# Performance work log

Hardware: AMD Instinct MI355X
Metric: run time of the kernel (lower is better)

Reference implementation:

```python
import jax, jax.numpy as jnp
import numpy as np

EPS_BN = 1e-5
EPS_ATT = 1e-9

def conv1x1(x, w, b=None):
    # x: [B,C,N], w: [O,C] -> [B,O,N]
    y = jnp.einsum('oc,bcn->bon', w, x)
    if b is not None:
        y = y + b[None, :, None]
    return y

def batchnorm1d(x, g, b):
    # training-mode BN over (batch, N) per channel, biased variance
    mean = jnp.mean(x, axis=(0, 2), keepdims=True)
    var = jnp.mean((x - mean) ** 2, axis=(0, 2), keepdims=True)
    xh = (x - mean) * jax.lax.rsqrt(var + EPS_BN)
    return xh * g[None, :, None] + b[None, :, None]

def sa_layer(x, xyz_emb, wqk, wv, bv, wt, bt, bng, bnb):
    # x, xyz_emb: [B,C,N]
    x = x + xyz_emb
    q = jnp.einsum('dc,bcn->bdn', wqk, x)      # [B,C/4,N] (shared weight)
    k = jnp.einsum('dc,bcn->bdn', wqk, x)
    v = conv1x1(x, wv, bv)                      # [B,C,N]
    attn = jnp.einsum('bdn,bdm->bnm', q, k)     # [B,N,N]: rows=queries n, cols=keys m
    attn = jax.nn.softmax(attn, axis=-1)
    attn = attn / (EPS_ATT + jnp.sum(attn, axis=1, keepdims=True))  # L1 renorm over dim=1
    x_r = jnp.einsum('bcn,bnm->bcm', v, attn)   # [B,C,N]
    x_r = jax.nn.relu(batchnorm1d(conv1x1(x - x_r, wt, bt), bng, bnb))
    return x + x_r

def setup_inputs() -> dict:
    key = jax.random.key(0)
    ks = jax.random.split(key, 12)
    B, C, N = 4, 128, 4096
    s = lambda fan: 1.0 / np.sqrt(fan)
    return {
        'x': jax.random.normal(ks[0], (B, C, N), jnp.float32),
        'xyz': jax.random.uniform(ks[1], (B, N, 3), jnp.float32),
        'conv1_w': jax.random.normal(ks[2], (C, C), jnp.float32) * s(C),
        'bn1_g': jnp.ones((C,), jnp.float32),
        'bn1_b': jnp.zeros((C,), jnp.float32),
        'pos_w': jax.random.normal(ks[3], (C, 3), jnp.float32) * s(3),
        'pos_b': jnp.zeros((C,), jnp.float32),
        'sa_wqk': jax.random.normal(ks[4], (5, C // 4, C), jnp.float32) * s(C),
        'sa_wv': jax.random.normal(ks[5], (5, C, C), jnp.float32) * s(C),
        'sa_bv': jnp.zeros((5, C), jnp.float32),
        'sa_wt': jax.random.normal(ks[6], (5, C, C), jnp.float32) * s(C),
        'sa_bt': jnp.zeros((5, C), jnp.float32),
        'sa_bng': jnp.ones((5, C), jnp.float32),
        'sa_bnb': jnp.zeros((5, C), jnp.float32),
    }

def reference(x, xyz, conv1_w, bn1_g, bn1_b, pos_w, pos_b,
              sa_wqk, sa_wv, sa_bv, sa_wt, sa_bt, sa_bng, sa_bnb):
    xyz_t = jnp.transpose(xyz, (0, 2, 1))           # [B,3,N]
    xyz_emb = conv1x1(xyz_t, pos_w, pos_b)          # [B,C,N]
    h = jax.nn.relu(batchnorm1d(conv1x1(x, conv1_w), bn1_g, bn1_b))
    outs = []
    for i in range(5):
        h = sa_layer(h, xyz_emb, sa_wqk[i], sa_wv[i], sa_bv[i],
                     sa_wt[i], sa_bt[i], sa_bng[i], sa_bnb[i])
        outs.append(h)
    return jnp.concatenate(outs, axis=1)            # [B,5C,N]
```

## Files before the change

kernel.cpp:

```cpp
#include <hip/hip_runtime.h>

#define kB 4
#define kC 128
#define kN 4096
#define kD 32
#define kL 5
#define kCO 640
#define kL2E 1.4426950408889634f

typedef float f32x4 __attribute__((ext_vector_type(4)));
typedef short bf16x4 __attribute__((ext_vector_type(4)));
typedef short bf16x8 __attribute__((ext_vector_type(8)));
typedef unsigned u32;
typedef u32 u32x4 __attribute__((ext_vector_type(4)));
typedef unsigned short u16;

__device__ __forceinline__ float bf2f(u16 u) {
  unsigned v = ((unsigned)u) << 16;
  return __builtin_bit_cast(float, v);
}
__device__ __forceinline__ u16 f2bf(float f) {
  unsigned u = __builtin_bit_cast(unsigned, f);
  u += 0x7fffu + ((u >> 16) & 1u);
  return (u16)(u >> 16);
}
__device__ __forceinline__ void split2(float v, u16& hi, u16& lo) {
  hi = f2bf(v);
  lo = f2bf(v - bf2f(hi));
}
__device__ __forceinline__ float fexp2(float x) {
#if __has_builtin(__builtin_amdgcn_exp2f)
  return __builtin_amdgcn_exp2f(x);
#else
  return exp2f(x);
#endif
}
__device__ __forceinline__ void splitpair(float a, float b, u32& hw, u32& lw) {
  u32 ua = __builtin_bit_cast(u32, a), ub = __builtin_bit_cast(u32, b);
  u32 uam = ua & 0xffff0000u, ubm = ub & 0xffff0000u;
  hw = (ua >> 16) | ubm;
  float la = a - __builtin_bit_cast(float, uam);
  float lb = b - __builtin_bit_cast(float, ubm);
  lw = (__builtin_bit_cast(u32, la) >> 16) | (__builtin_bit_cast(u32, lb) & 0xffff0000u);
}
__device__ __forceinline__ f32x4 mfma3(bf16x8 ah, bf16x8 al, bf16x8 bh, bf16x8 bl, f32x4 c) {
  c = __builtin_amdgcn_mfma_f32_16x16x32_bf16(ah, bh, c, 0, 0, 0);
  c = __builtin_amdgcn_mfma_f32_16x16x32_bf16(ah, bl, c, 0, 0, 0);
  c = __builtin_amdgcn_mfma_f32_16x16x32_bf16(al, bh, c, 0, 0, 0);
  return c;
}

__global__ void sentinel_kernel(float* out, float val, int total) {
  int i = blockIdx.x * 256 + threadIdx.x;
  if (i < total) out[i] = val;
}

__global__ void cvt_split_kernel(const float* __restrict__ src, u16* __restrict__ dh,
                                 u16* __restrict__ dl, int count) {
  int i = blockIdx.x * 256 + threadIdx.x;
  if (i < count) {
    u16 h, l;
    split2(src[i], h, l);
    dh[i] = h;
    dl[i] = l;
  }
}

__global__ __launch_bounds__(256) void prep_kernel(
    const float* __restrict__ h, long hstride, long hoff,
    u16* __restrict__ xh, u16* __restrict__ xl) {
  __shared__ float t[32][33];
  int n0 = blockIdx.x * 32, c0 = blockIdx.y * 32, b = blockIdx.z;
  int tx = threadIdx.x & 31, ty = threadIdx.x >> 5;
#pragma unroll
  for (int i = 0; i < 4; ++i) {
    int c = c0 + ty + i * 8;
    t[ty + i * 8][tx] = h[(size_t)b * hstride + hoff + (size_t)c * kN + n0 + tx];
  }
  __syncthreads();
#pragma unroll
  for (int i = 0; i < 4; ++i) {
    int n = n0 + ty + i * 8, c = c0 + tx;
    u16 hh, ll;
    split2(t[tx][ty + i * 8], hh, ll);
    size_t idx = ((size_t)b * kN + n) * kC + c;
    xh[idx] = hh;
    xl[idx] = ll;
  }
}

__global__ __launch_bounds__(320) void qv_kernel(
    const u16* __restrict__ xh, const u16* __restrict__ xl,
    const u16* __restrict__ wqkh, const u16* __restrict__ wqkl,
    const u16* __restrict__ wvh, const u16* __restrict__ wvl,
    const float* __restrict__ bv,
    u16* __restrict__ Qh, u16* __restrict__ Ql,
    u16* __restrict__ Vph, u16* __restrict__ Vpl) {
  __shared__ float vt[4][2][16][17];
  int wave = threadIdx.x >> 6, lane = threadIdx.x & 63;
  int b = blockIdx.y;
  int n0 = blockIdx.x * 16;
  int col = lane & 15, g = lane >> 4;
  f32x4 acc[2] = {};
  const u16* xrh = xh + ((size_t)b * kN + n0 + col) * kC + g * 8;
  const u16* xrl = xl + ((size_t)b * kN + n0 + col) * kC + g * 8;
#pragma unroll
  for (int kk = 0; kk < 4; ++kk) {
    bf16x8 bh = *(const bf16x8*)(xrh + kk * 32);
    bf16x8 bl = *(const bf16x8*)(xrl + kk * 32);
#pragma unroll
    for (int i = 0; i < 2; ++i) {
      int ot = wave * 2 + i;
      size_t wi = (ot < 2) ? ((size_t)(ot * 16 + col) * kC) : ((size_t)((ot - 2) * 16 + col) * kC);
      const u16* wsh = (ot < 2) ? (wqkh + wi) : (wvh + wi);
      const u16* wsl = (ot < 2) ? (wqkl + wi) : (wvl + wi);
      bf16x8 ah = *(const bf16x8*)(wsh + kk * 32 + g * 8);
      bf16x8 al = *(const bf16x8*)(wsl + kk * 32 + g * 8);
      acc[i] = mfma3(ah, al, bh, bl, acc[i]);
    }
  }
  if (wave > 0) {
#pragma unroll
    for (int i = 0; i < 2; ++i) {
      int ct = wave * 2 + i - 2;
#pragma unroll
      for (int r = 0; r < 4; ++r)
        vt[wave - 1][i][4 * g + r][col] = acc[i][r] + bv[ct * 16 + 4 * g + r];
    }
  }
  __syncthreads();
  if (wave == 0) {
#pragma unroll
    for (int i = 0; i < 2; ++i) {
#pragma unroll
      for (int r = 0; r < 4; ++r) {
        int d = i * 16 + 4 * g + r;
        u16 hh, ll;
        split2(acc[i][r], hh, ll);
        size_t idx = ((size_t)b * kN + n0 + col) * kD + d;
        Qh[idx] = hh;
        Ql[idx] = ll;
      }
    }
  } else {
    int nt = n0 >> 5, p = (n0 >> 4) & 1;
#pragma unroll
    for (int i = 0; i < 2; ++i) {
      int ct = wave * 2 + i - 2;
      bf16x4 vh4, vl4;
#pragma unroll
      for (int j = 0; j < 4; ++j) {
        float v = vt[wave - 1][i][col][4 * g + j];
        u16 hh, ll;
        split2(v, hh, ll);
        vh4[j] = (short)hh;
        vl4[j] = (short)ll;
      }
      size_t base = ((((size_t)b * (kN / 32) + nt) * 8 + ct) * 64 + lane) * 8 + p * 4;
      *(bf16x4*)(Vph + base) = vh4;
      *(bf16x4*)(Vpl + base) = vl4;
    }
  }
}

__global__ __launch_bounds__(256) void pass1_kernel(
    const u16* __restrict__ Qh, const u16* __restrict__ Ql,
    float* __restrict__ rm2, float* __restrict__ rinv) {
  __shared__ float mxs[4][16], sms[4][16];
  int wave = threadIdx.x >> 6, lane = threadIdx.x & 63;
  int b = blockIdx.y;
  int n0 = blockIdx.x * 16;
  int col = lane & 15, g = lane >> 4;
  const u16* qbh = Qh + (size_t)b * kN * kD;
  const u16* qbl = Ql + (size_t)b * kN * kD;
  bf16x8 ah = *(const bf16x8*)(qbh + (size_t)(n0 + col) * kD + g * 8);
  bf16x8 al = *(const bf16x8*)(qbl + (size_t)(n0 + col) * kD + g * 8);
  float mx[4] = {-3.0e38f, -3.0e38f, -3.0e38f, -3.0e38f};
  float sm[4] = {0.f, 0.f, 0.f, 0.f};
#pragma unroll 1
  for (int m0 = wave * 16; m0 < kN; m0 += 64) {
    bf16x8 bh = *(const bf16x8*)(qbh + (size_t)(m0 + col) * kD + g * 8);
    bf16x8 bl = *(const bf16x8*)(qbl + (size_t)(m0 + col) * kD + g * 8);
    f32x4 s = {};
    s = mfma3(ah, al, bh, bl, s);
#pragma unroll
    for (int r = 0; r < 4; ++r) {
      float nm = fmaxf(mx[r], s[r]);
      sm[r] = sm[r] * fexp2((mx[r] - nm) * kL2E) + fexp2((s[r] - nm) * kL2E);
      mx[r] = nm;
    }
  }
#pragma unroll
  for (int o = 1; o < 16; o <<= 1) {
#pragma unroll
    for (int r = 0; r < 4; ++r) {
      float Mo = __shfl_xor(mx[r], o, 64);
      float So = __shfl_xor(sm[r], o, 64);
      float nm = fmaxf(mx[r], Mo);
      sm[r] = sm[r] * fexp2((mx[r] - nm) * kL2E) + So * fexp2((Mo - nm) * kL2E);
      mx[r] = nm;
    }
  }
  if (col == 0) {
#pragma unroll
    for (int r = 0; r < 4; ++r) {
      mxs[wave][4 * g + r] = mx[r];
      sms[wave][4 * g + r] = sm[r];
    }
  }
  __syncthreads();
  if (threadIdx.x < 16) {
    int t = threadIdx.x;
    float M = mxs[0][t], S = sms[0][t];
#pragma unroll
    for (int w = 1; w < 4; ++w) {
      float Mo = mxs[w][t], So = sms[w][t];
      float nm = fmaxf(M, Mo);
      S = S * fexp2((M - nm) * kL2E) + So * fexp2((Mo - nm) * kL2E);
      M = nm;
    }
    rm2[(size_t)b * kN + n0 + t] = M * kL2E;
    rinv[(size_t)b * kN + n0 + t] = 1.0f / S;
  }
}

__global__ __launch_bounds__(256) void pass2_kernel(
    const u16* __restrict__ Qh, const u16* __restrict__ Ql,
    const u16* __restrict__ Vph, const u16* __restrict__ Vpl,
    const float* __restrict__ rm2, const float* __restrict__ rinv,
    const u16* __restrict__ xh, const u16* __restrict__ xl,
    u16* __restrict__ yth, u16* __restrict__ ytl) {
  __shared__ f32x4 accs[4][8][64];
  __shared__ float csl[2][4][16];
  int wave = threadIdx.x >> 6, lane = threadIdx.x & 63;
  int b = blockIdx.y;
  int m0 = blockIdx.x * 32;
  int col = lane & 15, g = lane >> 4;
  const u16* qbh = Qh + (size_t)b * kN * kD;
  const u16* qbl = Ql + (size_t)b * kN * kD;
  const float* rmb = rm2 + (size_t)b * kN;
  const float* rib = rinv + (size_t)b * kN;
  bf16x8 bmh0 = *(const bf16x8*)(qbh + (size_t)(m0 + col) * kD + g * 8);
  bf16x8 bml0 = *(const bf16x8*)(qbl + (size_t)(m0 + col) * kD + g * 8);
  bf16x8 bmh1 = *(const bf16x8*)(qbh + (size_t)(m0 + 16 + col) * kD + g * 8);
  bf16x8 bml1 = *(const bf16x8*)(qbl + (size_t)(m0 + 16 + col) * kD + g * 8);
  const u16* vbh = Vph + (size_t)b * (kN / 32) * 4096;
  const u16* vbl = Vpl + (size_t)b * (kN / 32) * 4096;
  f32x4 accA[8] = {}, accB[8] = {};
  float csA = 0.f, csB = 0.f;
#pragma unroll 1
  for (int nn = wave * 32; nn < kN; nn += 128) {
    bf16x8 ah0 = *(const bf16x8*)(qbh + (size_t)(nn + col) * kD + g * 8);
    bf16x8 al0 = *(const bf16x8*)(qbl + (size_t)(nn + col) * kD + g * 8);
    bf16x8 ah1 = *(const bf16x8*)(qbh + (size_t)(nn + 16 + col) * kD + g * 8);
    bf16x8 al1 = *(const bf16x8*)(qbl + (size_t)(nn + 16 + col) * kD + g * 8);
    f32x4 sA0 = {}, sA1 = {}, sB0 = {}, sB1 = {};
    sA0 = mfma3(ah0, al0, bmh0, bml0, sA0);
    sA1 = mfma3(ah1, al1, bmh0, bml0, sA1);
    sB0 = mfma3(ah0, al0, bmh1, bml1, sB0);
    sB1 = mfma3(ah1, al1, bmh1, bml1, sB1);
    float pA[8], pB[8];
#pragma unroll
    for (int r = 0; r < 4; ++r) {
      float e0 = rmb[nn + 4 * g + r], i0 = rib[nn + 4 * g + r];
      float e1 = rmb[nn + 16 + 4 * g + r], i1 = rib[nn + 16 + 4 * g + r];
      pA[r] = fexp2(sA0[r] * kL2E - e0) * i0;
      pA[r + 4] = fexp2(sA1[r] * kL2E - e1) * i1;
      pB[r] = fexp2(sB0[r] * kL2E - e0) * i0;
      pB[r + 4] = fexp2(sB1[r] * kL2E - e1) * i1;
      csA += pA[r] + pA[r + 4];
      csB += pB[r] + pB[r + 4];
    }
    u32x4 Ahw, Alw, Bhw, Blw;
#pragma unroll
    for (int k2 = 0; k2 < 4; ++k2) {
      u32 h0, l0, h1, l1;
      splitpair(pA[2 * k2], pA[2 * k2 + 1], h0, l0);
      splitpair(pB[2 * k2], pB[2 * k2 + 1], h1, l1);
      Ahw[k2] = h0; Alw[k2] = l0;
      Bhw[k2] = h1; Blw[k2] = l1;
    }
    bf16x8 bAh = __builtin_bit_cast(bf16x8, Ahw);
    bf16x8 bAl = __builtin_bit_cast(bf16x8, Alw);
    bf16x8 bBh = __builtin_bit_cast(bf16x8, Bhw);
    bf16x8 bBl = __builtin_bit_cast(bf16x8, Blw);
    size_t vtile = (size_t)(nn >> 5) * 4096;
#pragma unroll
    for (int ct = 0; ct < 8; ++ct) {
      size_t off = vtile + ((size_t)ct * 64 + lane) * 8;
      bf16x8 a8h = *(const bf16x8*)(vbh + off);
      bf16x8 a8l = *(const bf16x8*)(vbl + off);
      accA[ct] = mfma3(a8h, a8l, bAh, bAl, accA[ct]);
      accB[ct] = mfma3(a8h, a8l, bBh, bBl, accB[ct]);
    }
  }
  csA += __shfl_xor(csA, 16, 64);
  csA += __shfl_xor(csA, 32, 64);
  csB += __shfl_xor(csB, 16, 64);
  csB += __shfl_xor(csB, 32, 64);
  if (lane < 16) {
    csl[0][wave][lane] = csA;
    csl[1][wave][lane] = csB;
  }
#pragma unroll
  for (int ct = 0; ct < 8; ++ct) accs[wave][ct][lane] = accA[ct];
  __syncthreads();
  {
    float inv = 1.0f / (1e-9f + csl[0][0][col] + csl[0][1][col] + csl[0][2][col] + csl[0][3][col]);
    const u16* xrh = xh + ((size_t)b * kN + m0 + col) * kC;
    const u16* xrl = xl + ((size_t)b * kN + m0 + col) * kC;
#pragma unroll
    for (int i = 0; i < 2; ++i) {
      int ct = wave * 2 + i;
      f32x4 a = accs[0][ct][lane];
      a += accs[1][ct][lane];
      a += accs[2][ct][lane];
      a += accs[3][ct][lane];
      bf16x4 xvh = *(const bf16x4*)(xrh + ct * 16 + 4 * g);
      bf16x4 xvl = *(const bf16x4*)(xrl + ct * 16 + 4 * g);
#pragma unroll
      for (int r = 0; r < 4; ++r) {
        float xv = bf2f((u16)xvh[r]) + bf2f((u16)xvl[r]);
        float y = xv - a[r] * inv;
        u16 hh, ll;
        split2(y, hh, ll);
        size_t idx = ((size_t)b * kN + m0 + col) * kC + ct * 16 + 4 * g + r;
        yth[idx] = hh;
        ytl[idx] = ll;
      }
    }
  }
  __syncthreads();
#pragma unroll
  for (int ct = 0; ct < 8; ++ct) accs[wave][ct][lane] = accB[ct];
  __syncthreads();
  {
    float inv = 1.0f / (1e-9f + csl[1][0][col] + csl[1][1][col] + csl[1][2][col] + csl[1][3][col]);
    const u16* xrh = xh + ((size_t)b * kN + m0 + 16 + col) * kC;
    const u16* xrl = xl + ((size_t)b * kN + m0 + 16 + col) * kC;
#pragma unroll
    for (int i = 0; i < 2; ++i) {
      int ct = wave * 2 + i;
      f32x4 a = accs[0][ct][lane];
      a += accs[1][ct][lane];
      a += accs[2][ct][lane];
      a += accs[3][ct][lane];
      bf16x4 xvh = *(const bf16x4*)(xrh + ct * 16 + 4 * g);
      bf16x4 xvl = *(const bf16x4*)(xrl + ct * 16 + 4 * g);
#pragma unroll
      for (int r = 0; r < 4; ++r) {
        float xv = bf2f((u16)xvh[r]) + bf2f((u16)xvl[r]);
        float y = xv - a[r] * inv;
        u16 hh, ll;
        split2(y, hh, ll);
        size_t idx = ((size_t)b * kN + m0 + 16 + col) * kC + ct * 16 + 4 * g + r;
        yth[idx] = hh;
        ytl[idx] = ll;
      }
    }
  }
}

__global__ __launch_bounds__(256) void tconv_kernel(
    const u16* __restrict__ inh, const u16* __restrict__ inl,
    const u16* __restrict__ wh, const u16* __restrict__ wl,
    const float* __restrict__ bias, float* __restrict__ u,
    long ustride, long uoff) {
  int wave = threadIdx.x >> 6, lane = threadIdx.x & 63;
  int b = blockIdx.y;
  int n0 = blockIdx.x * 16;
  int col = lane & 15, g = lane >> 4;
  f32x4 acc[2] = {};
  const u16* xrh = inh + ((size_t)b * kN + n0 + col) * kC + g * 8;
  const u16* xrl = inl + ((size_t)b * kN + n0 + col) * kC + g * 8;
#pragma unroll
  for (int kk = 0; kk < 4; ++kk) {
    bf16x8 bh = *(const bf16x8*)(xrh + kk * 32);
    bf16x8 bl = *(const bf16x8*)(xrl + kk * 32);
#pragma unroll
    for (int i = 0; i < 2; ++i) {
      int ot = wave * 2 + i;
      bf16x8 ah = *(const bf16x8*)(wh + (size_t)(ot * 16 + col) * kC + kk * 32 + g * 8);
      bf16x8 al = *(const bf16x8*)(wl + (size_t)(ot * 16 + col) * kC + kk * 32 + g * 8);
      acc[i] = mfma3(ah, al, bh, bl, acc[i]);
    }
  }
#pragma unroll
  for (int i = 0; i < 2; ++i) {
    int ot = wave * 2 + i;
#pragma unroll
    for (int r = 0; r < 4; ++r) {
      int c = ot * 16 + 4 * g + r;
      float v = acc[i][r] + (bias ? bias[c] : 0.f);
      u[(size_t)b * ustride + uoff + (size_t)c * kN + n0 + col] = v;
    }
  }
}

__global__ __launch_bounds__(256) void bn_stats_kernel(const float* __restrict__ u,
                                                       long ustride, long uoff,
                                                       float* __restrict__ stat) {
  int c = blockIdx.x;
  __shared__ double reds[4], redss[4];
  double s = 0.0, ss = 0.0;
  for (int i = threadIdx.x; i < kB * kN; i += 256) {
    int b = i >> 12, n = i & (kN - 1);
    float v = u[(size_t)b * ustride + uoff + (size_t)c * kN + n];
    s += (double)v;
    ss += (double)v * (double)v;
  }
#pragma unroll
  for (int o = 1; o < 64; o <<= 1) {
    s += __shfl_xor(s, o, 64);
    ss += __shfl_xor(ss, o, 64);
  }
  int wid = threadIdx.x >> 6, lane = threadIdx.x & 63;
  if (lane == 0) { reds[wid] = s; redss[wid] = ss; }
  __syncthreads();
  if (threadIdx.x == 0) {
    double S = reds[0] + reds[1] + reds[2] + reds[3];
    double SS = redss[0] + redss[1] + redss[2] + redss[3];
    double mean = S / (double)(kB * kN);
    double var = SS / (double)(kB * kN) - mean * mean;
    if (var < 0.0) var = 0.0;
    stat[c] = (float)mean;
    stat[kC + c] = rsqrtf((float)var + 1e-5f);
  }
}

__global__ __launch_bounds__(256) void bnprep_kernel(
    const float* __restrict__ u, long ustride, long uoff,
    const float* __restrict__ stat,
    const float* __restrict__ g, const float* __restrict__ bb,
    const float* __restrict__ h, long hstride, long hoff, int use_res,
    const float* __restrict__ xyz, const float* __restrict__ pw,
    const float* __restrict__ pb,
    float* __restrict__ out, long ostride, long ooff,
    u16* __restrict__ xh, u16* __restrict__ xl) {
  __shared__ float t[32][33];
  int n0 = blockIdx.x * 32, c0 = blockIdx.y * 32, b = blockIdx.z;
  int tx = threadIdx.x & 31, ty = threadIdx.x >> 5;
  const float* xp = xyz + ((size_t)b * kN + n0 + tx) * 3;
  float xv0 = xp[0], xv1 = xp[1], xv2 = xp[2];
#pragma unroll
  for (int i = 0; i < 4; ++i) {
    int c = c0 + ty + i * 8;
    float e = pw[c * 3 + 0] * xv0 + pw[c * 3 + 1] * xv1 + pw[c * 3 + 2] * xv2 + pb[c];
    float y = (u[(size_t)b * ustride + uoff + (size_t)c * kN + n0 + tx] - stat[c]) *
                  stat[kC + c] * g[c] + bb[c];
    y = fmaxf(y, 0.f);
    if (use_res) y += h[(size_t)b * hstride + hoff + (size_t)c * kN + n0 + tx] + e;
    out[(size_t)b * ostride + ooff + (size_t)c * kN + n0 + tx] = y;
    t[ty + i * 8][tx] = y + e;
  }
  __syncthreads();
#pragma unroll
  for (int i = 0; i < 4; ++i) {
    int n = n0 + ty + i * 8, c = c0 + tx;
    u16 hh, ll;
    split2(t[tx][ty + i * 8], hh, ll);
    size_t idx = ((size_t)b * kN + n) * kC + c;
    xh[idx] = hh;
    xl[idx] = ll;
  }
}

extern "C" void kernel_launch(void* const* d_in, const int* in_sizes, int n_in,
                              void* d_out, int out_size, void* d_ws, size_t ws_size,
                              hipStream_t stream) {
  const float* x = (const float*)d_in[0];
  const float* xyz = (const float*)d_in[1];
  const float* conv1_w = (const float*)d_in[2];
  const float* bn1_g = (const float*)d_in[3];
  const float* bn1_b = (const float*)d_in[4];
  const float* pos_w = (const float*)d_in[5];
  const float* pos_b = (const float*)d_in[6];
  const float* sa_wqk = (const float*)d_in[7];
  const float* sa_wv = (const float*)d_in[8];
  const float* sa_bv = (const float*)d_in[9];
  const float* sa_wt = (const float*)d_in[10];
  const float* sa_bt = (const float*)d_in[11];
  const float* sa_bng = (const float*)d_in[12];
  const float* sa_bnb = (const float*)d_in[13];
  float* out = (float*)d_out;
  char* ws = (char*)d_ws;
  const size_t MB = (size_t)1 << 20;

  const size_t NEED = 28 * MB;
  if (ws_size < NEED) {
    float val = 100.0f + (float)(ws_size >> 20);
    sentinel_kernel<<<dim3((out_size + 255) / 256), dim3(256), 0, stream>>>(out, val, out_size);
    return;
  }

  u16* xh = (u16*)(ws);
  u16* xl = (u16*)(ws + 4 * MB);
  u16* yth = (u16*)(ws + 8 * MB);
  u16* ytl = (u16*)(ws + 12 * MB);
  u16* Vph = (u16*)(ws + 16 * MB);
  u16* Vpl = (u16*)(ws + 20 * MB);
  u16* Qh = (u16*)(ws + 24 * MB);
  u16* Ql = (u16*)(ws + 25 * MB);
  u16* wa = (u16*)(ws + 26 * MB);
  size_t woff = 0;
  u16* c1h = wa + woff; woff += 16384;
  u16* c1l = wa + woff; woff += 16384;
  u16* qkh = wa + woff; woff += 5 * 32 * 128;
  u16* qkl = wa + woff; woff += 5 * 32 * 128;
  u16* wvh = wa + woff; woff += 5 * 128 * 128;
  u16* wvl = wa + woff; woff += 5 * 128 * 128;
  u16* wth = wa + woff; woff += 5 * 128 * 128;
  u16* wtl = wa + woff; woff += 5 * 128 * 128;
  float* rm2 = (float*)(ws + 27 * MB);
  float* rinv = (float*)(ws + 27 * MB + 65536);
  float* stat = (float*)(ws + 27 * MB + 131072);

  dim3 blk(256);

  cvt_split_kernel<<<dim3(64), blk, 0, stream>>>(conv1_w, c1h, c1l, 16384);
  cvt_split_kernel<<<dim3(80), blk, 0, stream>>>(sa_wqk, qkh, qkl, 20480);
  cvt_split_kernel<<<dim3(320), blk, 0, stream>>>(sa_wv, wvh, wvl, 81920);
  cvt_split_kernel<<<dim3(320), blk, 0, stream>>>(sa_wt, wth, wtl, 81920);

  const long sbo = (long)kCO * kN;
  const long slice = (long)kC * kN;
  const long h0off = 4 * slice;

  prep_kernel<<<dim3(kN / 32, kC / 32, kB), blk, 0, stream>>>(x, slice, 0, xh, xl);
  tconv_kernel<<<dim3(kN / 16, kB), blk, 0, stream>>>(
      xh, xl, c1h, c1l, nullptr, out, sbo, 0);
  bn_stats_kernel<<<dim3(kC), blk, 0, stream>>>(out, sbo, 0, stat);
  bnprep_kernel<<<dim3(kN / 32, kC / 32, kB), blk, 0, stream>>>(
      out, sbo, 0, stat, bn1_g, bn1_b, nullptr, 0, 0, 0, xyz, pos_w, pos_b,
      out, sbo, h0off, xh, xl);

  long hoff = h0off;
  for (int i = 0; i < kL; ++i) {
    long uoff = (long)i * slice;
    qv_kernel<<<dim3(kN / 16, kB), dim3(320), 0, stream>>>(
        xh, xl, qkh + (size_t)i * kD * kC, qkl + (size_t)i * kD * kC,
        wvh + (size_t)i * kC * kC, wvl + (size_t)i * kC * kC,
        sa_bv + (size_t)i * kC, Qh, Ql, Vph, Vpl);
    pass1_kernel<<<dim3(kN / 16, kB), blk, 0, stream>>>(Qh, Ql, rm2, rinv);
    pass2_kernel<<<dim3(kN / 32, kB), blk, 0, stream>>>(
        Qh, Ql, Vph, Vpl, rm2, rinv, xh, xl, yth, ytl);
    tconv_kernel<<<dim3(kN / 16, kB), blk, 0, stream>>>(
        yth, ytl, wth + (size_t)i * kC * kC, wtl + (size_t)i * kC * kC,
        sa_bt + (size_t)i * kC, out, sbo, uoff);
    bn_stats_kernel<<<dim3(kC), blk, 0, stream>>>(out, sbo, uoff, stat);
    bnprep_kernel<<<dim3(kN / 32, kC / 32, kB), blk, 0, stream>>>(
        out, sbo, uoff, stat, sa_bng + (size_t)i * kC, sa_bnb + (size_t)i * kC,
        out, sbo, hoff, 1, xyz, pos_w, pos_b, out, sbo, uoff, xh, xl);
    hoff = uoff;
  }
}
```

Before: 893.9 us.

## Widen attention pass tiles to reuse key/value loads across more query rows

```diff
diff --git a/kernel.cpp b/kernel.cpp
--- a/kernel.cpp
+++ b/kernel.cpp
@@ -166,34 +166,41 @@
 __global__ __launch_bounds__(256) void pass1_kernel(
     const u16* __restrict__ Qh, const u16* __restrict__ Ql,
     float* __restrict__ rm2, float* __restrict__ rinv) {
-  __shared__ float mxs[4][16], sms[4][16];
+  __shared__ float mxs[4][32], sms[4][32];
   int wave = threadIdx.x >> 6, lane = threadIdx.x & 63;
   int b = blockIdx.y;
-  int n0 = blockIdx.x * 16;
+  int n0 = blockIdx.x * 32;
   int col = lane & 15, g = lane >> 4;
   const u16* qbh = Qh + (size_t)b * kN * kD;
   const u16* qbl = Ql + (size_t)b * kN * kD;
-  bf16x8 ah = *(const bf16x8*)(qbh + (size_t)(n0 + col) * kD + g * 8);
-  bf16x8 al = *(const bf16x8*)(qbl + (size_t)(n0 + col) * kD + g * 8);
-  float mx[4] = {-3.0e38f, -3.0e38f, -3.0e38f, -3.0e38f};
-  float sm[4] = {0.f, 0.f, 0.f, 0.f};
+  bf16x8 ah0 = *(const bf16x8*)(qbh + (size_t)(n0 + col) * kD + g * 8);
+  bf16x8 al0 = *(const bf16x8*)(qbl + (size_t)(n0 + col) * kD + g * 8);
+  bf16x8 ah1 = *(const bf16x8*)(qbh + (size_t)(n0 + 16 + col) * kD + g * 8);
+  bf16x8 al1 = *(const bf16x8*)(qbl + (size_t)(n0 + 16 + col) * kD + g * 8);
+  float mx[8], sm[8];
+#pragma unroll
+  for (int r = 0; r < 8; ++r) { mx[r] = -3.0e38f; sm[r] = 0.f; }
 #pragma unroll 1
   for (int m0 = wave * 16; m0 < kN; m0 += 64) {
     bf16x8 bh = *(const bf16x8*)(qbh + (size_t)(m0 + col) * kD + g * 8);
     bf16x8 bl = *(const bf16x8*)(qbl + (size_t)(m0 + col) * kD + g * 8);
-    f32x4 s = {};
-    s = mfma3(ah, al, bh, bl, s);
+    f32x4 s0 = {}, s1 = {};
+    s0 = mfma3(ah0, al0, bh, bl, s0);
+    s1 = mfma3(ah1, al1, bh, bl, s1);
 #pragma unroll
     for (int r = 0; r < 4; ++r) {
-      float nm = fmaxf(mx[r], s[r]);
-      sm[r] = sm[r] * fexp2((mx[r] - nm) * kL2E) + fexp2((s[r] - nm) * kL2E);
-      mx[r] = nm;
+      float nm0 = fmaxf(mx[r], s0[r]);
+      sm[r] = sm[r] * fexp2((mx[r] - nm0) * kL2E) + fexp2((s0[r] - nm0) * kL2E);
+      mx[r] = nm0;
+      float nm1 = fmaxf(mx[r + 4], s1[r]);
+      sm[r + 4] = sm[r + 4] * fexp2((mx[r + 4] - nm1) * kL2E) + fexp2((s1[r] - nm1) * kL2E);
+      mx[r + 4] = nm1;
     }
   }
 #pragma unroll
   for (int o = 1; o < 16; o <<= 1) {
 #pragma unroll
-    for (int r = 0; r < 4; ++r) {
+    for (int r = 0; r < 8; ++r) {
       float Mo = __shfl_xor(mx[r], o, 64);
       float So = __shfl_xor(sm[r], o, 64);
       float nm = fmaxf(mx[r], Mo);
@@ -206,10 +213,12 @@
     for (int r = 0; r < 4; ++r) {
       mxs[wave][4 * g + r] = mx[r];
       sms[wave][4 * g + r] = sm[r];
+      mxs[wave][16 + 4 * g + r] = mx[r + 4];
+      sms[wave][16 + 4 * g + r] = sm[r + 4];
     }
   }
   __syncthreads();
-  if (threadIdx.x < 16) {
+  if (threadIdx.x < 32) {
     int t = threadIdx.x;
     float M = mxs[0][t], S = sms[0][t];
 #pragma unroll
@@ -224,141 +233,133 @@
   }
 }
 
-__global__ __launch_bounds__(256) void pass2_kernel(
+#define PFRAG(S0, S1, CS, BPH, BPL)                       \
+  {                                                       \
+    float p[8];                                           \
+    _Pragma("unroll") for (int r = 0; r < 4; ++r) {       \
+      p[r] = fexp2(S0[r] * kL2E - e0[r]) * i0[r];         \
+      p[r + 4] = fexp2(S1[r] * kL2E - e1[r]) * i1[r];     \
+      CS += p[r] + p[r + 4];                              \
+    }                                                     \
+    u32x4 hw, lw;                                         \
+    _Pragma("unroll") for (int k2 = 0; k2 < 4; ++k2) {    \
+      u32 hh, llw;                                        \
+      splitpair(p[2 * k2], p[2 * k2 + 1], hh, llw);       \
+      hw[k2] = hh;                                        \
+      lw[k2] = llw;                                       \
+    }                                                     \
+    BPH = __builtin_bit_cast(bf16x8, hw);                 \
+    BPL = __builtin_bit_cast(bf16x8, lw);                 \
+  }
+
+__global__ __launch_bounds__(512) void pass2_kernel(
     const u16* __restrict__ Qh, const u16* __restrict__ Ql,
     const u16* __restrict__ Vph, const u16* __restrict__ Vpl,
     const float* __restrict__ rm2, const float* __restrict__ rinv,
     const u16* __restrict__ xh, const u16* __restrict__ xl,
     u16* __restrict__ yth, u16* __restrict__ ytl) {
-  __shared__ f32x4 accs[4][8][64];
-  __shared__ float csl[2][4][16];
+  __shared__ f32x4 accs[8][8][64];
+  __shared__ float csl[4][8][16];
   int wave = threadIdx.x >> 6, lane = threadIdx.x & 63;
   int b = blockIdx.y;
-  int m0 = blockIdx.x * 32;
+  int m0 = blockIdx.x * 64;
   int col = lane & 15, g = lane >> 4;
   const u16* qbh = Qh + (size_t)b * kN * kD;
   const u16* qbl = Ql + (size_t)b * kN * kD;
   const float* rmb = rm2 + (size_t)b * kN;
   const float* rib = rinv + (size_t)b * kN;
-  bf16x8 bmh0 = *(const bf16x8*)(qbh + (size_t)(m0 + col) * kD + g * 8);
-  bf16x8 bml0 = *(const bf16x8*)(qbl + (size_t)(m0 + col) * kD + g * 8);
-  bf16x8 bmh1 = *(const bf16x8*)(qbh + (size_t)(m0 + 16 + col) * kD + g * 8);
-  bf16x8 bml1 = *(const bf16x8*)(qbl + (size_t)(m0 + 16 + col) * kD + g * 8);
+  bf16x8 bmh[4], bml[4];
+#pragma unroll
+  for (int f = 0; f < 4; ++f) {
+    bmh[f] = *(const bf16x8*)(qbh + (size_t)(m0 + 16 * f + col) * kD + g * 8);
+    bml[f] = *(const bf16x8*)(qbl + (size_t)(m0 + 16 * f + col) * kD + g * 8);
+  }
   const u16* vbh = Vph + (size_t)b * (kN / 32) * 4096;
   const u16* vbl = Vpl + (size_t)b * (kN / 32) * 4096;
-  f32x4 accA[8] = {}, accB[8] = {};
-  float csA = 0.f, csB = 0.f;
+  f32x4 acc0[8] = {}, acc1[8] = {}, acc2[8] = {}, acc3[8] = {};
+  float cs0 = 0.f, cs1 = 0.f, cs2 = 0.f, cs3 = 0.f;
 #pragma unroll 1
-  for (int nn = wave * 32; nn < kN; nn += 128) {
+  for (int nn = wave * 32; nn < kN; nn += 256) {
     bf16x8 ah0 = *(const bf16x8*)(qbh + (size_t)(nn + col) * kD + g * 8);
     bf16x8 al0 = *(const bf16x8*)(qbl + (size_t)(nn + col) * kD + g * 8);
     bf16x8 ah1 = *(const bf16x8*)(qbh + (size_t)(nn + 16 + col) * kD + g * 8);
     bf16x8 al1 = *(const bf16x8*)(qbl + (size_t)(nn + 16 + col) * kD + g * 8);
-    f32x4 sA0 = {}, sA1 = {}, sB0 = {}, sB1 = {};
-    sA0 = mfma3(ah0, al0, bmh0, bml0, sA0);
-    sA1 = mfma3(ah1, al1, bmh0, bml0, sA1);
-    sB0 = mfma3(ah0, al0, bmh1, bml1, sB0);
-    sB1 = mfma3(ah1, al1, bmh1, bml1, sB1);
-    float pA[8], pB[8];
+    f32x4 s00 = {}, s01 = {}, s10 = {}, s11 = {}, s20 = {}, s21 = {}, s30 = {}, s31 = {};
+    s00 = mfma3(ah0, al0, bmh[0], bml[0], s00);
+    s01 = mfma3(ah1, al1, bmh[0], bml[0], s01);
+    s10 = mfma3(ah0, al0, bmh[1], bml[1], s10);
+    s11 = mfma3(ah1, al1, bmh[1], bml[1], s11);
+    s20 = mfma3(ah0, al0, bmh[2], bml[2], s20);
+    s21 = mfma3(ah1, al1, bmh[2], bml[2], s21);
+    s30 = mfma3(ah0, al0, bmh[3], bml[3], s30);
+    s31 = mfma3(ah1, al1, bmh[3], bml[3], s31);
+    float e0[4], i0[4], e1[4], i1[4];
 #pragma unroll
     for (int r = 0; r < 4; ++r) {
-      float e0 = rmb[nn + 4 * g + r], i0 = rib[nn + 4 * g + r];
-      float e1 = rmb[nn + 16 + 4 * g + r], i1 = rib[nn + 16 + 4 * g + r];
-      pA[r] = fexp2(sA0[r] * kL2E - e0) * i0;
-      pA[r + 4] = fexp2(sA1[r] * kL2E - e1) * i1;
-      pB[r] = fexp2(sB0[r] * kL2E - e0) * i0;
-      pB[r + 4] = fexp2(sB1[r] * kL2E - e1) * i1;
-      csA += pA[r] + pA[r + 4];
-      csB += pB[r] + pB[r + 4];
-    }
-    u32x4 Ahw, Alw, Bhw, Blw;
-#pragma unroll
-    for (int k2 = 0; k2 < 4; ++k2) {
-      u32 h0, l0, h1, l1;
-      splitpair(pA[2 * k2], pA[2 * k2 + 1], h0, l0);
-      splitpair(pB[2 * k2], pB[2 * k2 + 1], h1, l1);
-      Ahw[k2] = h0; Alw[k2] = l0;
-      Bhw[k2] = h1; Blw[k2] = l1;
-    }
-    bf16x8 bAh = __builtin_bit_cast(bf16x8, Ahw);
-    bf16x8 bAl = __builtin_bit_cast(bf16x8, Alw);
-    bf16x8 bBh = __builtin_bit_cast(bf16x8, Bhw);
-    bf16x8 bBl = __builtin_bit_cast(bf16x8, Blw);
+      e0[r] = rmb[nn + 4 * g + r];
+      i0[r] = rib[nn + 4 * g + r];
+      e1[r] = rmb[nn + 16 + 4 * g + r];
+      i1[r] = rib[nn + 16 + 4 * g + r];
+    }
+    bf16x8 bph0, bpl0, bph1, bpl1, bph2, bpl2, bph3, bpl3;
+    PFRAG(s00, s01, cs0, bph0, bpl0)
+    PFRAG(s10, s11, cs1, bph1, bpl1)
+    PFRAG(s20, s21, cs2, bph2, bpl2)
+    PFRAG(s30, s31, cs3, bph3, bpl3)
     size_t vtile = (size_t)(nn >> 5) * 4096;
 #pragma unroll
     for (int ct = 0; ct < 8; ++ct) {
       size_t off = vtile + ((size_t)ct * 64 + lane) * 8;
       bf16x8 a8h = *(const bf16x8*)(vbh + off);
       bf16x8 a8l = *(const bf16x8*)(vbl + off);
-      accA[ct] = mfma3(a8h, a8l, bAh, bAl, accA[ct]);
-      accB[ct] = mfma3(a8h, a8l, bBh, bBl, accB[ct]);
-    }
-  }
-  csA += __shfl_xor(csA, 16, 64);
-  csA += __shfl_xor(csA, 32, 64);
-  csB += __shfl_xor(csB, 16, 64);
-  csB += __shfl_xor(csB, 32, 64);
+      acc0[ct] = mfma3(a8h, a8l, bph0, bpl0, acc0[ct]);
+      acc1[ct] = mfma3(a8h, a8l, bph1, bpl1, acc1[ct]);
+      acc2[ct] = mfma3(a8h, a8l, bph2, bpl2, acc2[ct]);
+      acc3[ct] = mfma3(a8h, a8l, bph3, bpl3, acc3[ct]);
+    }
+  }
+  cs0 += __shfl_xor(cs0, 16, 64); cs0 += __shfl_xor(cs0, 32, 64);
+  cs1 += __shfl_xor(cs1, 16, 64); cs1 += __shfl_xor(cs1, 32, 64);
+  cs2 += __shfl_xor(cs2, 16, 64); cs2 += __shfl_xor(cs2, 32, 64);
+  cs3 += __shfl_xor(cs3, 16, 64); cs3 += __shfl_xor(cs3, 32, 64);
   if (lane < 16) {
-    csl[0][wave][lane] = csA;
-    csl[1][wave][lane] = csB;
-  }
-#pragma unroll
-  for (int ct = 0; ct < 8; ++ct) accs[wave][ct][lane] = accA[ct];
-  __syncthreads();
-  {
-    float inv = 1.0f / (1e-9f + csl[0][0][col] + csl[0][1][col] + csl[0][2][col] + csl[0][3][col]);
-    const u16* xrh = xh + ((size_t)b * kN + m0 + col) * kC;
-    const u16* xrl = xl + ((size_t)b * kN + m0 + col) * kC;
-#pragma unroll
-    for (int i = 0; i < 2; ++i) {
-      int ct = wave * 2 + i;
-      f32x4 a = accs[0][ct][lane];
-      a += accs[1][ct][lane];
-      a += accs[2][ct][lane];
-      a += accs[3][ct][lane];
-      bf16x4 xvh = *(const bf16x4*)(xrh + ct * 16 + 4 * g);
-      bf16x4 xvl = *(const bf16x4*)(xrl + ct * 16 + 4 * g);
-#pragma unroll
-      for (int r = 0; r < 4; ++r) {
-        float xv = bf2f((u16)xvh[r]) + bf2f((u16)xvl[r]);
-        float y = xv - a[r] * inv;
-        u16 hh, ll;
-        split2(y, hh, ll);
-        size_t idx = ((size_t)b * kN + m0 + col) * kC + ct * 16 + 4 * g + r;
-        yth[idx] = hh;
-        ytl[idx] = ll;
-      }
-    }
-  }
-  __syncthreads();
-#pragma unroll
-  for (int ct = 0; ct < 8; ++ct) accs[wave][ct][lane] = accB[ct];
-  __syncthreads();
-  {
-    float inv = 1.0f / (1e-9f + csl[1][0][col] + csl[1][1][col] + csl[1][2][col] + csl[1][3][col]);
-    const u16* xrh = xh + ((size_t)b * kN + m0 + 16 + col) * kC;
-    const u16* xrl = xl + ((size_t)b * kN + m0 + 16 + col) * kC;
-#pragma unroll
-    for (int i = 0; i < 2; ++i) {
-      int ct = wave * 2 + i;
-      f32x4 a = accs[0][ct][lane];
-      a += accs[1][ct][lane];
-      a += accs[2][ct][lane];
-      a += accs[3][ct][lane];
-      bf16x4 xvh = *(const bf16x4*)(xrh + ct * 16 + 4 * g);
-      bf16x4 xvl = *(const bf16x4*)(xrl + ct * 16 + 4 * g);
-#pragma unroll
-      for (int r = 0; r < 4; ++r) {
-        float xv = bf2f((u16)xvh[r]) + bf2f((u16)xvl[r]);
-        float y = xv - a[r] * inv;
-        u16 hh, ll;
-        split2(y, hh, ll);
-        size_t idx = ((size_t)b * kN + m0 + 16 + col) * kC + ct * 16 + 4 * g + r;
-        yth[idx] = hh;
-        ytl[idx] = ll;
-      }
-    }
-  }
+    csl[0][wave][lane] = cs0;
+    csl[1][wave][lane] = cs1;
+    csl[2][wave][lane] = cs2;
+    csl[3][wave][lane] = cs3;
+  }
+#define PHASE(F, ACC)                                                            \
+  {                                                                              \
+    _Pragma("unroll") for (int ct = 0; ct < 8; ++ct)                             \
+        accs[wave][ct][lane] = ACC[ct];                                          \
+    __syncthreads();                                                             \
+    float csum = 0.f;                                                            \
+    _Pragma("unroll") for (int w = 0; w < 8; ++w) csum += csl[F][w][col];        \
+    float inv = 1.0f / (1e-9f + csum);                                           \
+    int row = m0 + 16 * F + col;                                                 \
+    int ct = wave;                                                               \
+    f32x4 a = accs[0][ct][lane];                                                 \
+    _Pragma("unroll") for (int w = 1; w < 8; ++w) a += accs[w][ct][lane];        \
+    const u16* xrh = xh + ((size_t)b * kN + row) * kC;                           \
+    const u16* xrl = xl + ((size_t)b * kN + row) * kC;                           \
+    bf16x4 xvh = *(const bf16x4*)(xrh + ct * 16 + 4 * g);                        \
+    bf16x4 xvl = *(const bf16x4*)(xrl + ct * 16 + 4 * g);                        \
+    _Pragma("unroll") for (int r = 0; r < 4; ++r) {                              \
+      float xv = bf2f((u16)xvh[r]) + bf2f((u16)xvl[r]);                          \
+      float y = xv - a[r] * inv;                                                 \
+      u16 hh, ll;                                                                \
+      split2(y, hh, ll);                                                         \
+      size_t idx = ((size_t)b * kN + row) * kC + ct * 16 + 4 * g + r;            \
+      yth[idx] = hh;                                                             \
+      ytl[idx] = ll;                                                             \
+    }                                                                            \
+    __syncthreads();                                                             \
+  }
+  PHASE(0, acc0)
+  PHASE(1, acc1)
+  PHASE(2, acc2)
+  PHASE(3, acc3)
+#undef PHASE
 }
 
 __global__ __launch_bounds__(256) void tconv_kernel(
@@ -541,8 +542,8 @@
         xh, xl, qkh + (size_t)i * kD * kC, qkl + (size_t)i * kD * kC,
         wvh + (size_t)i * kC * kC, wvl + (size_t)i * kC * kC,
         sa_bv + (size_t)i * kC, Qh, Ql, Vph, Vpl);
-    pass1_kernel<<<dim3(kN / 16, kB), blk, 0, stream>>>(Qh, Ql, rm2, rinv);
-    pass2_kernel<<<dim3(kN / 32, kB), blk, 0, stream>>>(
+    pass1_kernel<<<dim3(kN / 32, kB), blk, 0, stream>>>(Qh, Ql, rm2, rinv);
+    pass2_kernel<<<dim3(kN / 64, kB), dim3(512), 0, stream>>>(
         Qh, Ql, Vph, Vpl, rm2, rinv, xh, xl, yth, ytl);
     tconv_kernel<<<dim3(kN / 16, kB), blk, 0, stream>>>(
         yth, ytl, wth + (size_t)i * kC * kC, wtl + (size_t)i * kC * kC,
```

Measured after the change: 1.014 ms. +13.4%, slower.
